# Kernel tuning notes

Hardware: AMD Instinct MI355X
Metric: run time of the kernel (lower is better)

## Reference

```python
import jax, jax.numpy as jnp
import numpy as np

B, T, E = 4, 2048, 512      # batch, seq_len, embedding_dim
H, D = 8, 64                # n_heads, head_size


def setup_inputs() -> dict:
    key = jax.random.key(0)
    ks = jax.random.split(key, 8)
    rn = lambda k, sh, sc=1.0: jax.random.normal(k, sh, dtype=jnp.float32) * sc
    return {
        "x": rn(ks[0], (B, T, E)),
        "k": rn(ks[1], (B, T, E)),
        "q": rn(ks[2], (B, T, E)),
        "v": rn(ks[3], (B, T, E)),
        # per-head Q/K/V projection weights, stacked: [H, D, E] (bias=False as in nanoGPT-style heads)
        "Wq": rn(ks[4], (H, D, E), E ** -0.5),
        "Wk": rn(ks[5], (H, D, E), E ** -0.5),
        "Wv": rn(ks[6], (H, D, E), E ** -0.5),
        # output projection Linear(H*D -> E)
        "Wo": rn(ks[7], (E, H * D), (H * D) ** -0.5),
        "bo": jnp.zeros((E,), jnp.float32),
    }


def reference(x, k, q, v, Wq, Wk, Wv, Wo, bo):
    # batched equivalent of the per-head Python loop: one einsum per Q/K/V
    qh = jnp.einsum('bte,hde->bhtd', q, Wq)   # [B,H,T,D]
    kh = jnp.einsum('bse,hde->bhsd', k, Wk)
    vh = jnp.einsum('bse,hde->bhsd', v, Wv)
    scores = jnp.einsum('bhtd,bhsd->bhts', qh, kh) * (D ** -0.5)
    Tq = x.shape[1]
    causal = jnp.tril(jnp.ones((Tq, Tq), dtype=bool))  # masked=True: tril mask
    scores = jnp.where(causal, scores, -jnp.inf)
    wei = jax.nn.softmax(scores, axis=-1)              # dropout=0.0 -> identity
    out = jnp.einsum('bhts,bhsd->bhtd', wei, vh)       # [B,H,T,D]
    out = out.transpose(0, 2, 1, 3).reshape(x.shape[0], Tq, H * D)  # concat heads
    return out @ Wo.T + bo                              # final projection
```

## Files before the change

kernel.cpp:

```cpp
#include <hip/hip_runtime.h>
#include <hip/hip_bf16.h>
#include <cstdint>
#include <cstddef>

#define Bb 4
#define Tt 2048
#define Ee 512
#define Hh 8
#define Dd 64
#define HD 512
#define BT 8192

typedef __bf16 bf16x8 __attribute__((ext_vector_type(8)));
typedef __bf16 bf16x4 __attribute__((ext_vector_type(4)));
typedef short s16x4 __attribute__((ext_vector_type(4)));
typedef float f32x4 __attribute__((ext_vector_type(4)));

__device__ __forceinline__ f32x4 mfma16(bf16x8 a, bf16x8 b, f32x4 c) {
  return __builtin_amdgcn_mfma_f32_16x16x32_bf16(a, b, c, 0, 0, 0);
}

__device__ __forceinline__ s16x4 as_s16x4(bf16x4 v) {
  union { bf16x4 b; s16x4 s; } u; u.b = v; return u.s;
}

__device__ __forceinline__ f32x4 mfma16k16(bf16x4 a, bf16x4 b, f32x4 c) {
#if defined(__HIP_DEVICE_COMPILE__)
  return __builtin_amdgcn_mfma_f32_16x16x16bf16_1k(as_s16x4(a), as_s16x4(b), c, 0, 0, 0);
#else
  (void)a; (void)b;
  return c;
#endif
}

typedef __attribute__((address_space(3))) uint32_t lds_u32_t;
typedef const __attribute__((address_space(1))) uint32_t glb_u32_t;
__device__ __forceinline__ void gload16(const void* g, void* l) {
  __builtin_amdgcn_global_load_lds((glb_u32_t*)g, (lds_u32_t*)l, 16, 0, 0);
}

__global__ void cvt_w_kernel(const float* __restrict__ wq, const float* __restrict__ wk,
                             const float* __restrict__ wv, const float* __restrict__ wo,
                             __bf16* __restrict__ dst) {
  int id = blockIdx.x * 256 + threadIdx.x;
  int r = id & 127;
  int lgg = (id >> 7) & 3;
  int p = (id >> 9) & 15;
  int cb = (id >> 13) & 3;
  int m = id >> 15;
  const float* src = (m == 0) ? wq : (m == 1) ? wk : (m == 2) ? wv : wo;
  const float* s = src + (size_t)(cb * 128 + r) * 512 + p * 32 + lgg * 8;
  float4 f0 = *(const float4*)s;
  float4 f1 = *(const float4*)(s + 4);
  bf16x8 o;
  o[0] = (__bf16)f0.x; o[1] = (__bf16)f0.y; o[2] = (__bf16)f0.z; o[3] = (__bf16)f0.w;
  o[4] = (__bf16)f1.x; o[5] = (__bf16)f1.y; o[6] = (__bf16)f1.z; o[7] = (__bf16)f1.w;
  *(bf16x8*)(dst + (size_t)m * 262144 + cb * 65536 + p * 4096 + lgg * 1024 + r * 8) = o;
}

__global__ __launch_bounds__(256)
void gemm_qkv_kernel(const float* __restrict__ Aq, const float* __restrict__ Ak,
                     const float* __restrict__ Av, const __bf16* __restrict__ Wall,
                     __bf16* __restrict__ qh, __bf16* __restrict__ kh, __bf16* __restrict__ vt) {
  const int id = blockIdx.x;
  const int xcd = id & 7, s = id >> 3;
  const int bx = s & 3;
  const int pair = xcd + 8 * (s >> 2);
  const int by = pair & 63;
  const int pz = pair >> 6;

  const float* A = (pz == 0) ? Aq : (pz == 1) ? Ak : Av;
  const char* Bw = (const char*)(Wall + (size_t)pz * 262144 + (size_t)bx * 65536);
  const int row0 = by * 128;
  const int col0 = bx * 128;

  __shared__ __align__(16) __bf16 As[128 * 32];
  __shared__ __align__(16) __bf16 Bs[128 * 32];
  char* As8 = (char*)As;
  char* Bs8 = (char*)Bs;

  const int tid = threadIdx.x;
  const int l = tid & 63, w = tid >> 6;
  const int ln = l & 15, lg = l >> 4;
  const int wr = (w >> 1) * 64, wc = (w & 1) * 64;

  const int sr = tid >> 1;
  const int sce = (tid & 1) * 16;
  const int sbyte = sr * 64 + sce * 2;
  const int swz = (sr & 7) << 4;

  f32x4 acc[4][4] = {};

  const float* agbase = A + (size_t)(row0 + sr) * Ee + sce;
  float4 a0 = *(const float4*)(agbase);
  float4 a1 = *(const float4*)(agbase + 4);
  float4 a2 = *(const float4*)(agbase + 8);
  float4 a3 = *(const float4*)(agbase + 12);

  for (int ktp = 0; ktp < 16; ktp++) {
    bf16x8 c0, c1;
    c0[0] = (__bf16)a0.x; c0[1] = (__bf16)a0.y; c0[2] = (__bf16)a0.z; c0[3] = (__bf16)a0.w;
    c0[4] = (__bf16)a1.x; c0[5] = (__bf16)a1.y; c0[6] = (__bf16)a1.z; c0[7] = (__bf16)a1.w;
    c1[0] = (__bf16)a2.x; c1[1] = (__bf16)a2.y; c1[2] = (__bf16)a2.z; c1[3] = (__bf16)a2.w;
    c1[4] = (__bf16)a3.x; c1[5] = (__bf16)a3.y; c1[6] = (__bf16)a3.z; c1[7] = (__bf16)a3.w;
    __syncthreads();
    {
      const char* pb = Bw + ktp * 8192;
      gload16(pb + w * 2048 + l * 16, Bs8 + w * 2048);
      gload16(pb + w * 2048 + 1024 + l * 16, Bs8 + w * 2048 + 1024);
    }
    *(bf16x8*)(As8 + ((sbyte) ^ swz)) = c0;
    *(bf16x8*)(As8 + ((sbyte + 16) ^ swz)) = c1;
    if (ktp < 15) {
      const float* ag = agbase + (ktp + 1) * 32;
      a0 = *(const float4*)(ag);
      a1 = *(const float4*)(ag + 4);
      a2 = *(const float4*)(ag + 8);
      a3 = *(const float4*)(ag + 12);
    }
    __builtin_amdgcn_sched_barrier(0);
    __syncthreads();
    bf16x8 af[4], bfr[4];
#pragma unroll
    for (int mi = 0; mi < 4; mi++) {
      int r = wr + mi * 16 + ln;
      af[mi] = *(const bf16x8*)(As8 + ((r * 64 + lg * 16) ^ ((r & 7) << 4)));
    }
#pragma unroll
    for (int ni = 0; ni < 4; ni++) {
      int rr = wc + ni * 16 + ln;
      bfr[ni] = *(const bf16x8*)(Bs8 + lg * 2048 + rr * 16);
    }
#pragma unroll
    for (int mi = 0; mi < 4; mi++)
#pragma unroll
      for (int ni = 0; ni < 4; ni++)
        acc[mi][ni] = mfma16(af[mi], bfr[ni], acc[mi][ni]);
  }

  const float sc = (pz == 0) ? 0.18033688011112042f : 1.0f;
#pragma unroll
  for (int mi = 0; mi < 4; mi++) {
    const int rowb = row0 + wr + mi * 16 + lg * 4;
    const int bb = rowb >> 11;
    const int t0 = rowb & (Tt - 1);
#pragma unroll
    for (int ni = 0; ni < 4; ni++) {
      const int colb = col0 + wc + ni * 16 + ln;
      const int hh = colb >> 6;
      const int dd = colb & 63;
      if (pz == 2) {
        bf16x4 pk;
#pragma unroll
        for (int r = 0; r < 4; r++) pk[r] = (__bf16)acc[mi][ni][r];
        *(bf16x4*)(vt + (size_t)(bb * Hh + hh) * 131072 +
                   (t0 >> 6) * 4096 + ((t0 & 63) >> 2) * 256 + dd * 4) = pk;
      } else {
        __bf16* dstp = (pz == 0 ? qh : kh) + ((size_t)(bb * Hh + hh) * Tt + t0) * Dd + dd;
#pragma unroll
        for (int r = 0; r < 4; r++) dstp[(size_t)r * Dd] = (__bf16)(acc[mi][ni][r] * sc);
      }
    }
  }
}

__global__ __launch_bounds__(256)
void attn1_kernel(const __bf16* __restrict__ qh, const __bf16* __restrict__ kh,
                  const __bf16* __restrict__ vt, __bf16* __restrict__ opart,
                  float* __restrict__ lpart) {
  const int j = blockIdx.x;
  const int xcd = j & 7, slot = j >> 3;
  const int ck = slot & 1;
  const int p = (slot >> 1) & 15;
  const int bhi = slot >> 5;
  const int bh = xcd + 8 * bhi;

  __shared__ __align__(16) char Kb[2][8192];
  __shared__ __align__(16) char Vb[2][8192];

  const int tid = threadIdx.x;
  const int l = tid & 63, w = tid >> 6;
  const int ln = l & 15, lg = l >> 4;

  const char* Kg = (const char*)(kh + (size_t)bh * Tt * Dd);
  const char* Vg = (const char*)(vt + (size_t)bh * 131072);
  const __bf16* Q = qh + (size_t)bh * Tt * Dd;

  const int rsub = l >> 3;
  const int csw = ((l & 7) ^ rsub) * 16;
  const int krow = w * 16 + rsub;
  const int cb = ck * 32 + bh;

  bf16x4 ones;
#pragma unroll
  for (int r = 0; r < 4; r++) ones[r] = (__bf16)1.0f;

#pragma unroll 1
  for (int ph = 0; ph < 2; ph++) {
    const int qt = ph ? (31 - p) : p;
    const int nlo = qt + 1;
    const int mid = (nlo + 1) >> 1;
    const int tb = ck ? mid : 0;
    const int te = ck ? nlo : mid;
    const int qr = qt * 64 + w * 16;

    __syncthreads();

    f32x4 oacc[4] = {};
    f32x4 lsum = {};

    if (tb < te) {
      {
        const char* kt = Kg + (size_t)tb * 8192;
        const char* vtile = Vg + (size_t)tb * 8192;
        char* kb = (char*)Kb[0] + w * 2048;
        char* vb = (char*)Vb[0] + w * 2048;
        gload16(kt + krow * 128 + csw, kb);
        gload16(kt + (krow + 8) * 128 + csw, kb + 1024);
        gload16(vtile + w * 2048 + l * 16, vb);
        gload16(vtile + w * 2048 + 1024 + l * 16, vb + 1024);
      }

      bf16x8 qf[2];
#pragma unroll
      for (int kk = 0; kk < 2; kk++)
        qf[kk] = *(const bf16x8*)(Q + (size_t)(qr + ln) * Dd + kk * 32 + lg * 8);

      for (int st = tb; st < te; ++st) {
        const int cur = (st - tb) & 1;
        asm volatile("s_waitcnt vmcnt(0)" ::: "memory");
        __builtin_amdgcn_s_barrier();
        __builtin_amdgcn_sched_barrier(0);
        if (st + 1 < te) {
          const char* kt = Kg + (size_t)(st + 1) * 8192;
          const char* vtile = Vg + (size_t)(st + 1) * 8192;
          char* kb = (char*)Kb[cur ^ 1] + w * 2048;
          char* vb = (char*)Vb[cur ^ 1] + w * 2048;
          gload16(kt + krow * 128 + csw, kb);
          gload16(kt + (krow + 8) * 128 + csw, kb + 1024);
          gload16(vtile + w * 2048 + l * 16, vb);
          gload16(vtile + w * 2048 + 1024 + l * 16, vb + 1024);
        }
        const char* KB = Kb[cur];
        const char* VB = Vb[cur];
        const int s0 = st * 64;

        f32x4 sacc[4] = {};
        __builtin_amdgcn_s_setprio(1);
#pragma unroll
        for (int kk = 0; kk < 2; kk++) {
#pragma unroll
          for (int ni = 0; ni < 4; ni++) {
            bf16x8 kf = *(const bf16x8*)(KB + (ni * 16 + ln) * 128 + (((kk * 4 + lg) ^ (ln & 7)) * 16));
            sacc[ni] = mfma16(kf, qf[kk], sacc[ni]);
          }
        }
        __builtin_amdgcn_s_setprio(0);

        if (st == qt) {
#pragma unroll
          for (int ni = 0; ni < 4; ni++)
#pragma unroll
            for (int r = 0; r < 4; r++)
              if ((s0 + ni * 16 + lg * 4 + r) > (qr + ln)) sacc[ni][r] = -1e30f;
        }

        bf16x4 pk[4];
#pragma unroll
        for (int ni = 0; ni < 4; ni++)
#pragma unroll
          for (int r = 0; r < 4; r++)
            pk[ni][r] = (__bf16)__builtin_amdgcn_exp2f(sacc[ni][r]);

        __builtin_amdgcn_s_setprio(1);
#pragma unroll
        for (int nd = 0; nd < 4; nd++) {
          const char* vrow = VB + (nd * 16 + ln) * 8 + lg * 512;
#pragma unroll
          for (int ni = 0; ni < 4; ni++) {
            bf16x4 vfr = *(const bf16x4*)(vrow + ni * 2048);
            oacc[nd] = mfma16k16(vfr, pk[ni], oacc[nd]);
          }
        }
#pragma unroll
        for (int ni = 0; ni < 4; ni++)
          lsum = mfma16k16(ones, pk[ni], lsum);
        __builtin_amdgcn_s_setprio(0);
      }
    }

#pragma unroll
    for (int nd = 0; nd < 4; nd++) {
      bf16x4 ov;
#pragma unroll
      for (int r = 0; r < 4; r++) ov[r] = (__bf16)oacc[nd][r];
      *(bf16x4*)(opart + ((size_t)cb * Tt + qr + ln) * 64 + nd * 16 + lg * 4) = ov;
    }
    if (l < 16) {
      lpart[(size_t)cb * Tt + qr + l] = lsum[0];
    }
  }
}

__global__ __launch_bounds__(256)
void gemm_out_kernel(const __bf16* __restrict__ opart, const float* __restrict__ lpart,
                     const __bf16* __restrict__ Wall, const float* __restrict__ bo,
                     float* __restrict__ out) {
  const int id = blockIdx.x;
  const int xcd = id & 7, s = id >> 3;
  const int bx = s & 3;
  const int by = xcd + 8 * (s >> 2);

  const int row0 = by * 64;
  const int col0 = bx * 128;
  const char* Bw = (const char*)(Wall + (size_t)3 * 262144 + (size_t)bx * 65536);

  __shared__ __align__(16) __bf16 As[64 * 32];
  __shared__ __align__(16) __bf16 Bs[128 * 32];
  char* As8 = (char*)As;
  char* Bs8 = (char*)Bs;

  const int tid = threadIdx.x;
  const int l = tid & 63, w = tid >> 6;
  const int ln = l & 15, lg = l >> 4;
  const int wr = (w >> 1) * 32, wc = (w & 1) * 64;

  const int sr = tid >> 2;
  const int q = tid & 3;
  const int abyte = sr * 64 + q * 16;
  const int aswz = (sr & 7) << 4;

  const int srow = row0 + sr;
  const int b = srow >> 11, t = srow & (Tt - 1);

  f32x4 acc[2][4] = {};

  int c = q * 8;
  int h = c >> 6;
  size_t i0 = ((size_t)(b * Hh + h) * Tt + t) * 64 + (c & 63);
  bf16x8 v0 = *(const bf16x8*)(opart + i0);
  bf16x8 v1 = *(const bf16x8*)(opart + i0 + (size_t)32 * Tt * 64);
  float l0 = lpart[(size_t)(b * Hh + h) * Tt + t];
  float l1 = lpart[(size_t)(32 + b * Hh + h) * Tt + t];

  for (int ktp = 0; ktp < 16; ktp++) {
    float rden = 1.0f / (l0 + l1);
    bf16x8 c0;
#pragma unroll
    for (int e = 0; e < 8; e++)
      c0[e] = (__bf16)(((float)v0[e] + (float)v1[e]) * rden);
    __syncthreads();
    {
      const char* pb = Bw + ktp * 8192;
      gload16(pb + w * 2048 + l * 16, Bs8 + w * 2048);
      gload16(pb + w * 2048 + 1024 + l * 16, Bs8 + w * 2048 + 1024);
    }
    *(bf16x8*)(As8 + (abyte ^ aswz)) = c0;
    if (ktp < 15) {
      c = (ktp + 1) * 32 + q * 8;
      h = c >> 6;
      i0 = ((size_t)(b * Hh + h) * Tt + t) * 64 + (c & 63);
      v0 = *(const bf16x8*)(opart + i0);
      v1 = *(const bf16x8*)(opart + i0 + (size_t)32 * Tt * 64);
      l0 = lpart[(size_t)(b * Hh + h) * Tt + t];
      l1 = lpart[(size_t)(32 + b * Hh + h) * Tt + t];
    }
    __builtin_amdgcn_sched_barrier(0);
    __syncthreads();
    bf16x8 af[2], bfr[4];
#pragma unroll
    for (int mi = 0; mi < 2; mi++) {
      int r = wr + mi * 16 + ln;
      af[mi] = *(const bf16x8*)(As8 + ((r * 64 + lg * 16) ^ ((r & 7) << 4)));
    }
#pragma unroll
    for (int ni = 0; ni < 4; ni++) {
      int rr = wc + ni * 16 + ln;
      bfr[ni] = *(const bf16x8*)(Bs8 + lg * 2048 + rr * 16);
    }
#pragma unroll
    for (int mi = 0; mi < 2; mi++)
#pragma unroll
      for (int ni = 0; ni < 4; ni++)
        acc[mi][ni] = mfma16(af[mi], bfr[ni], acc[mi][ni]);
  }

#pragma unroll
  for (int mi = 0; mi < 2; mi++) {
    const int rowb = row0 + wr + mi * 16 + lg * 4;
#pragma unroll
    for (int ni = 0; ni < 4; ni++) {
      const int col = col0 + wc + ni * 16 + ln;
      const float bias = bo[col];
#pragma unroll
      for (int r = 0; r < 4; r++)
        out[(size_t)(rowb + r) * Ee + col] = acc[mi][ni][r] + bias;
    }
  }
}

extern "C" void kernel_launch(void* const* d_in, const int* in_sizes, int n_in,
                              void* d_out, int out_size, void* d_ws, size_t ws_size,
                              hipStream_t stream) {
  (void)in_sizes; (void)n_in; (void)out_size; (void)ws_size;
  const float* kin = (const float*)d_in[1];
  const float* qin = (const float*)d_in[2];
  const float* vin = (const float*)d_in[3];
  const float* Wq = (const float*)d_in[4];
  const float* Wk = (const float*)d_in[5];
  const float* Wv = (const float*)d_in[6];
  const float* Wo = (const float*)d_in[7];
  const float* bo = (const float*)d_in[8];
  float* out = (float*)d_out;

  __bf16* wall = (__bf16*)d_ws;
  __bf16* qh = wall + (size_t)1048576;
  __bf16* kh = qh + (size_t)4194304;
  __bf16* vt = kh + (size_t)4194304;
  __bf16* opart = vt + (size_t)4194304;
  float* lpart = (float*)(opart + (size_t)8388608);

  cvt_w_kernel<<<dim3(512), dim3(256), 0, stream>>>(Wq, Wk, Wv, Wo, wall);
  gemm_qkv_kernel<<<dim3(768), dim3(256), 0, stream>>>(qin, kin, vin, wall, qh, kh, vt);
  attn1_kernel<<<dim3(1024), dim3(256), 0, stream>>>(qh, kh, vt, opart, lpart);
  gemm_out_kernel<<<dim3(512), dim3(256), 0, stream>>>(opart, lpart, wall, bo, out);
}
```

Measured before the change: 80.40 us.

## Process paired causal query tiles concurrently in 512-thread attention blocks sharing K/V tiles

The attention kernel now runs both query tiles of a causal pair (p and 31-p) at the same time, using two 4-wave groups in one 512-thread block, instead of handling them one after the other. Each K/V tile is loaded once into LDS and shared by both groups. The key split also changes from contiguous halves to interleaved tiles (st = ck, ck+2, ...). This is meant to halve K/V global loads for the short tile and remove the serial phase loop and its barriers. In exchange, the short-tile group sits idle once its causal range ends, and the larger block may lower occupancy.

```diff
diff --git a/kernel.cpp b/kernel.cpp
--- a/kernel.cpp
+++ b/kernel.cpp
@@ -164,14 +164,14 @@
   }
 }
 
-__global__ __launch_bounds__(256)
+__global__ __launch_bounds__(512)
 void attn1_kernel(const __bf16* __restrict__ qh, const __bf16* __restrict__ kh,
                   const __bf16* __restrict__ vt, __bf16* __restrict__ opart,
                   float* __restrict__ lpart) {
   const int j = blockIdx.x;
   const int xcd = j & 7, slot = j >> 3;
   const int ck = slot & 1;
-  const int p = (slot >> 1) & 15;
+  const int pp = (slot >> 1) & 15;
   const int bhi = slot >> 5;
   const int bh = xcd + 8 * bhi;
 
@@ -181,6 +181,7 @@
   const int tid = threadIdx.x;
   const int l = tid & 63, w = tid >> 6;
   const int ln = l & 15, lg = l >> 4;
+  const int grp = w >> 2, wg = w & 3;
 
   const char* Kg = (const char*)(kh + (size_t)bh * Tt * Dd);
   const char* Vg = (const char*)(vt + (size_t)bh * 131072);
@@ -188,117 +189,101 @@
 
   const int rsub = l >> 3;
   const int csw = ((l & 7) ^ rsub) * 16;
-  const int krow = w * 16 + rsub;
   const int cb = ck * 32 + bh;
 
+  const int qt = grp ? (31 - pp) : pp;
+  const int n = qt + 1;
+  const int nmax = 32 - pp;
+  const int qr = qt * 64 + wg * 16;
+
   bf16x4 ones;
 #pragma unroll
   for (int r = 0; r < 4; r++) ones[r] = (__bf16)1.0f;
 
-#pragma unroll 1
-  for (int ph = 0; ph < 2; ph++) {
-    const int qt = ph ? (31 - p) : p;
-    const int nlo = qt + 1;
-    const int mid = (nlo + 1) >> 1;
-    const int tb = ck ? mid : 0;
-    const int te = ck ? nlo : mid;
-    const int qr = qt * 64 + w * 16;
-
-    __syncthreads();
-
-    f32x4 oacc[4] = {};
-    f32x4 lsum = {};
-
-    if (tb < te) {
-      {
-        const char* kt = Kg + (size_t)tb * 8192;
-        const char* vtile = Vg + (size_t)tb * 8192;
-        char* kb = (char*)Kb[0] + w * 2048;
-        char* vb = (char*)Vb[0] + w * 2048;
-        gload16(kt + krow * 128 + csw, kb);
-        gload16(kt + (krow + 8) * 128 + csw, kb + 1024);
-        gload16(vtile + w * 2048 + l * 16, vb);
-        gload16(vtile + w * 2048 + 1024 + l * 16, vb + 1024);
+  f32x4 oacc[4] = {};
+  f32x4 lsum = {};
+
+  {
+    const char* kt = Kg + (size_t)ck * 8192;
+    const char* vtile = Vg + (size_t)ck * 8192;
+    gload16(kt + (w * 8 + rsub) * 128 + csw, (char*)Kb[0] + w * 1024);
+    gload16(vtile + w * 1024 + l * 16, (char*)Vb[0] + w * 1024);
+  }
+
+  bf16x8 qf[2];
+#pragma unroll
+  for (int kk = 0; kk < 2; kk++)
+    qf[kk] = *(const bf16x8*)(Q + (size_t)(qr + ln) * Dd + kk * 32 + lg * 8);
+
+  for (int st = ck; st < nmax; st += 2) {
+    const int cur = ((st - ck) >> 1) & 1;
+    asm volatile("s_waitcnt vmcnt(0)" ::: "memory");
+    __builtin_amdgcn_s_barrier();
+    __builtin_amdgcn_sched_barrier(0);
+    if (st + 2 < nmax) {
+      const char* kt = Kg + (size_t)(st + 2) * 8192;
+      const char* vtile = Vg + (size_t)(st + 2) * 8192;
+      gload16(kt + (w * 8 + rsub) * 128 + csw, (char*)Kb[cur ^ 1] + w * 1024);
+      gload16(vtile + w * 1024 + l * 16, (char*)Vb[cur ^ 1] + w * 1024);
+    }
+    if (st < n) {
+      const char* KB = Kb[cur];
+      const char* VB = Vb[cur];
+      const int s0 = st * 64;
+
+      f32x4 sacc[4] = {};
+      __builtin_amdgcn_s_setprio(1);
+#pragma unroll
+      for (int kk = 0; kk < 2; kk++) {
+#pragma unroll
+        for (int ni = 0; ni < 4; ni++) {
+          bf16x8 kf = *(const bf16x8*)(KB + (ni * 16 + ln) * 128 + (((kk * 4 + lg) ^ (ln & 7)) * 16));
+          sacc[ni] = mfma16(kf, qf[kk], sacc[ni]);
+        }
       }
-
-      bf16x8 qf[2];
-#pragma unroll
-      for (int kk = 0; kk < 2; kk++)
-        qf[kk] = *(const bf16x8*)(Q + (size_t)(qr + ln) * Dd + kk * 32 + lg * 8);
-
-      for (int st = tb; st < te; ++st) {
-        const int cur = (st - tb) & 1;
-        asm volatile("s_waitcnt vmcnt(0)" ::: "memory");
-        __builtin_amdgcn_s_barrier();
-        __builtin_amdgcn_sched_barrier(0);
-        if (st + 1 < te) {
-          const char* kt = Kg + (size_t)(st + 1) * 8192;
-          const char* vtile = Vg + (size_t)(st + 1) * 8192;
-          char* kb = (char*)Kb[cur ^ 1] + w * 2048;
-          char* vb = (char*)Vb[cur ^ 1] + w * 2048;
-          gload16(kt + krow * 128 + csw, kb);
-          gload16(kt + (krow + 8) * 128 + csw, kb + 1024);
-          gload16(vtile + w * 2048 + l * 16, vb);
-          gload16(vtile + w * 2048 + 1024 + l * 16, vb + 1024);
+      __builtin_amdgcn_s_setprio(0);
+
+      if (st == qt) {
+#pragma unroll
+        for (int ni = 0; ni < 4; ni++)
+#pragma unroll
+          for (int r = 0; r < 4; r++)
+            if ((s0 + ni * 16 + lg * 4 + r) > (qr + ln)) sacc[ni][r] = -1e30f;
+      }
+
+      bf16x4 pk[4];
+#pragma unroll
+      for (int ni = 0; ni < 4; ni++)
+#pragma unroll
+        for (int r = 0; r < 4; r++)
+          pk[ni][r] = (__bf16)__builtin_amdgcn_exp2f(sacc[ni][r]);
+
+      __builtin_amdgcn_s_setprio(1);
+#pragma unroll
+      for (int nd = 0; nd < 4; nd++) {
+        const char* vrow = VB + (nd * 16 + ln) * 8 + lg * 512;
+#pragma unroll
+        for (int ni = 0; ni < 4; ni++) {
+          bf16x4 vfr = *(const bf16x4*)(vrow + ni * 2048);
+          oacc[nd] = mfma16k16(vfr, pk[ni], oacc[nd]);
         }
-        const char* KB = Kb[cur];
-        const char* VB = Vb[cur];
-        const int s0 = st * 64;
-
-        f32x4 sacc[4] = {};
-        __builtin_amdgcn_s_setprio(1);
-#pragma unroll
-        for (int kk = 0; kk < 2; kk++) {
-#pragma unroll
-          for (int ni = 0; ni < 4; ni++) {
-            bf16x8 kf = *(const bf16x8*)(KB + (ni * 16 + ln) * 128 + (((kk * 4 + lg) ^ (ln & 7)) * 16));
-            sacc[ni] = mfma16(kf, qf[kk], sacc[ni]);
-          }
-        }
-        __builtin_amdgcn_s_setprio(0);
-
-        if (st == qt) {
-#pragma unroll
-          for (int ni = 0; ni < 4; ni++)
-#pragma unroll
-            for (int r = 0; r < 4; r++)
-              if ((s0 + ni * 16 + lg * 4 + r) > (qr + ln)) sacc[ni][r] = -1e30f;
-        }
-
-        bf16x4 pk[4];
-#pragma unroll
-        for (int ni = 0; ni < 4; ni++)
-#pragma unroll
-          for (int r = 0; r < 4; r++)
-            pk[ni][r] = (__bf16)__builtin_amdgcn_exp2f(sacc[ni][r]);
-
-        __builtin_amdgcn_s_setprio(1);
-#pragma unroll
-        for (int nd = 0; nd < 4; nd++) {
-          const char* vrow = VB + (nd * 16 + ln) * 8 + lg * 512;
-#pragma unroll
-          for (int ni = 0; ni < 4; ni++) {
-            bf16x4 vfr = *(const bf16x4*)(vrow + ni * 2048);
-            oacc[nd] = mfma16k16(vfr, pk[ni], oacc[nd]);
-          }
-        }
-#pragma unroll
-        for (int ni = 0; ni < 4; ni++)
-          lsum = mfma16k16(ones, pk[ni], lsum);
-        __builtin_amdgcn_s_setprio(0);
       }
-    }
-
-#pragma unroll
-    for (int nd = 0; nd < 4; nd++) {
-      bf16x4 ov;
-#pragma unroll
-      for (int r = 0; r < 4; r++) ov[r] = (__bf16)oacc[nd][r];
-      *(bf16x4*)(opart + ((size_t)cb * Tt + qr + ln) * 64 + nd * 16 + lg * 4) = ov;
-    }
-    if (l < 16) {
-      lpart[(size_t)cb * Tt + qr + l] = lsum[0];
-    }
+#pragma unroll
+      for (int ni = 0; ni < 4; ni++)
+        lsum = mfma16k16(ones, pk[ni], lsum);
+      __builtin_amdgcn_s_setprio(0);
+    }
+  }
+
+#pragma unroll
+  for (int nd = 0; nd < 4; nd++) {
+    bf16x4 ov;
+#pragma unroll
+    for (int r = 0; r < 4; r++) ov[r] = (__bf16)oacc[nd][r];
+    *(bf16x4*)(opart + ((size_t)cb * Tt + qr + ln) * 64 + nd * 16 + lg * 4) = ov;
+  }
+  if (l < 16) {
+    lpart[(size_t)cb * Tt + qr + l] = lsum[0];
   }
 }
 
@@ -422,6 +407,6 @@
 
   cvt_w_kernel<<<dim3(512), dim3(256), 0, stream>>>(Wq, Wk, Wv, Wo, wall);
   gemm_qkv_kernel<<<dim3(768), dim3(256), 0, stream>>>(qin, kin, vin, wall, qh, kh, vt);
-  attn1_kernel<<<dim3(1024), dim3(256), 0, stream>>>(qh, kh, vt, opart, lpart);
+  attn1_kernel<<<dim3(1024), dim3(512), 0, stream>>>(qh, kh, vt, opart, lpart);
   gemm_out_kernel<<<dim3(512), dim3(256), 0, stream>>>(opart, lpart, wall, bo, out);
 }
```

Measured after the change: 81.87 us. Within noise of the previous version (+1.8%).
